# Kernel optimization log

Hardware: AMD Instinct MI355X
Metric: run time of the kernel (lower is better)

## Reference

```python
import jax, jax.numpy as jnp
import numpy as np

B, T, N, P2, K_S = 8, 64, 128, 256, 64

def setup_inputs() -> dict:
    key = jax.random.key(0)
    k1, k2, k3, k4 = jax.random.split(key, 4)
    x = jax.random.normal(k1, (B, T, N, P2), dtype=jnp.float32)
    W_Q = jax.random.uniform(k2, (P2, K_S), dtype=jnp.float32)
    W_K = jax.random.uniform(k3, (P2, K_S), dtype=jnp.float32)
    W_V = jax.random.uniform(k4, (P2, P2), dtype=jnp.float32)
    return {"x": x, "W_Q": W_Q, "W_K": W_K, "W_V": W_V}

def reference(x, W_Q, W_K, W_V):
    # x: [B, T, N, P2]
    q = jnp.einsum('btnp,pk->btnk', x, W_Q)          # [B,T,N,K_S]
    k = jnp.einsum('btnp,pk->btnk', x, W_K)          # [B,T,N,K_S]
    v = jnp.einsum('btnp,pq->btnq', x, W_V)          # [B,T,N,P2]
    scale = jnp.sqrt(jnp.asarray(K_S, dtype=x.dtype))
    scores = jnp.einsum('btik,btjk->btij', q, k) / scale  # [B,T,N,N]
    # NOTE: original uses nn.Softmax(dim=1) -> softmax over the T axis.
    attn = jax.nn.softmax(scores, axis=1)
    return jnp.einsum('btij,btjq->btiq', attn, v)    # [B,T,N,P2]
```

## Files before the change

### kernel.cpp

```cpp
#include <hip/hip_runtime.h>
#include <hip/hip_bf16.h>

#define Bv 8
#define Tv 64
#define Nv 128
#define P2v 256
#define KSv 64

typedef __attribute__((ext_vector_type(8))) short bf8;
typedef __attribute__((ext_vector_type(4))) float f4;

#define MFMA16(a, b, c) __builtin_amdgcn_mfma_f32_16x16x32_bf16((a), (b), (c), 0, 0, 0)

__device__ __forceinline__ unsigned short f2bf(float f) {
  unsigned u = __float_as_uint(f);
  return (unsigned short)((u + 0x7fffu + ((u >> 16) & 1u)) >> 16);
}
__device__ __forceinline__ float bf2f(unsigned short h) {
  return __uint_as_float(((unsigned)h) << 16);
}

__device__ __forceinline__ int swz64(int r, int c) {
  return r * 64 + ((((c >> 3)) ^ (r & 7)) << 3) + (c & 7);
}
__device__ __forceinline__ int swz32(int r, int c) {
  return r * 32 + ((((c >> 3)) ^ (r & 3)) << 3) + (c & 7);
}
__device__ __forceinline__ int swz128(int r, int c) {
  return r * 128 + ((((c >> 3)) ^ (r & 7)) << 3) + (c & 7);
}

__global__ __launch_bounds__(256) void prep_w_kernel(
    const float* __restrict__ Wq, const float* __restrict__ Wk,
    const float* __restrict__ Wv, unsigned short* __restrict__ wqh,
    unsigned short* __restrict__ wql, unsigned short* __restrict__ wkh,
    unsigned short* __restrict__ wkl, unsigned short* __restrict__ wvf) {
  const int e = blockIdx.x * 256 + threadIdx.x;
  if (e < 32768) {
    const float* W = (e < 16384) ? Wq : Wk;
    unsigned short* oh = (e < 16384) ? wqh : wkh;
    unsigned short* ol = (e < 16384) ? wql : wkl;
    const int t = e & 16383;
    const int jj = t & 7, lane = (t >> 3) & 63, nt = (t >> 9) & 3, pt = t >> 11;
    const int p = pt * 32 + 8 * (lane >> 4) + jj;
    const int n = nt * 16 + (lane & 15);
    const float v = W[p * KSv + n];
    const unsigned short h = f2bf(v);
    oh[t] = h;
    ol[t] = f2bf(v - bf2f(h));
  } else {
    const int t = e - 32768;
    const int jj = t & 7, lane = (t >> 3) & 63, nt = (t >> 9) & 15, pt = t >> 13;
    const int p = pt * 32 + 8 * (lane >> 4) + jj;
    const int q = nt * 16 + (lane & 15);
    wvf[t] = f2bf(Wv[p * P2v + q]);
  }
}

__global__ __launch_bounds__(512) void qk_kernel(
    const float* __restrict__ x, const unsigned short* __restrict__ wqh,
    const unsigned short* __restrict__ wql,
    const unsigned short* __restrict__ wkh,
    const unsigned short* __restrict__ wkl, float* __restrict__ S) {
  __shared__ alignas(16) unsigned short xh_l[Nv * 32];
  __shared__ alignas(16) unsigned short xl_l[Nv * 32];
  __shared__ alignas(16) unsigned short qh_l[Nv * KSv];
  __shared__ alignas(16) unsigned short ql_l[Nv * KSv];
  __shared__ alignas(16) unsigned short kh_l[Nv * KSv];
  __shared__ alignas(16) unsigned short kl_l[Nv * KSv];
  const int bt = blockIdx.x;
  const float* __restrict__ X = x + (size_t)bt * (Nv * P2v);
  const int tid = threadIdx.x, lane = tid & 63, wid = tid >> 6;
  const int lg = lane >> 4, lr = lane & 15;
  const bool isQ = (wid < 4);
  const int nt = wid & 3;
  const unsigned short* __restrict__ wh = isQ ? wqh : wkh;
  const unsigned short* __restrict__ wl = isQ ? wql : wkl;

  const f4 zero = {0.f, 0.f, 0.f, 0.f};
  f4 acc[8];
#pragma unroll
  for (int rt = 0; rt < 8; ++rt) acc[rt] = zero;

  const int srow = tid >> 2;
  const int sp = (tid & 3) * 8;
  const float* __restrict__ Xrow = X + srow * P2v + sp;

  float4 pv0 = *(const float4*)(Xrow);
  float4 pv1 = *(const float4*)(Xrow + 4);
  bf8 pwh = *(const bf8*)(wh + (nt * 64 + lane) * 8);
  bf8 pwl = *(const bf8*)(wl + (nt * 64 + lane) * 8);

  for (int c = 0; c < 8; ++c) {
    ushort4 h0, l0, h1, l1;
    h0.x = f2bf(pv0.x); l0.x = f2bf(pv0.x - bf2f(h0.x));
    h0.y = f2bf(pv0.y); l0.y = f2bf(pv0.y - bf2f(h0.y));
    h0.z = f2bf(pv0.z); l0.z = f2bf(pv0.z - bf2f(h0.z));
    h0.w = f2bf(pv0.w); l0.w = f2bf(pv0.w - bf2f(h0.w));
    h1.x = f2bf(pv1.x); l1.x = f2bf(pv1.x - bf2f(h1.x));
    h1.y = f2bf(pv1.y); l1.y = f2bf(pv1.y - bf2f(h1.y));
    h1.z = f2bf(pv1.z); l1.z = f2bf(pv1.z - bf2f(h1.z));
    h1.w = f2bf(pv1.w); l1.w = f2bf(pv1.w - bf2f(h1.w));
    const bf8 cwh = pwh, cwl = pwl;

    __syncthreads();
    const int off = swz32(srow, sp);
    *(ushort4*)(xh_l + off) = h0;
    *(ushort4*)(xh_l + off + 4) = h1;
    *(ushort4*)(xl_l + off) = l0;
    *(ushort4*)(xl_l + off + 4) = l1;

    if (c < 7) {
      pv0 = *(const float4*)(Xrow + (c + 1) * 32);
      pv1 = *(const float4*)(Xrow + (c + 1) * 32 + 4);
      const int wo = (((c + 1) * 4 + nt) * 64 + lane) * 8;
      pwh = *(const bf8*)(wh + wo);
      pwl = *(const bf8*)(wl + wo);
    }
    __syncthreads();
#pragma unroll
    for (int rt = 0; rt < 8; ++rt) {
      const int xoff = swz32(rt * 16 + lr, lg * 8);
      const bf8 xh = *(const bf8*)(xh_l + xoff);
      const bf8 xl = *(const bf8*)(xl_l + xoff);
      acc[rt] = MFMA16(xh, cwh, acc[rt]);
      acc[rt] = MFMA16(xh, cwl, acc[rt]);
      acc[rt] = MFMA16(xl, cwh, acc[rt]);
    }
  }

  unsigned short* const oh = isQ ? qh_l : kh_l;
  unsigned short* const ol = isQ ? ql_l : kl_l;
#pragma unroll
  for (int rt = 0; rt < 8; ++rt) {
#pragma unroll
    for (int rr = 0; rr < 4; ++rr) {
      const int i = rt * 16 + 4 * lg + rr;
      const int ks = nt * 16 + lr;
      const int off = swz64(i, ks);
      const float v = acc[rt][rr];
      const unsigned short h = f2bf(v);
      oh[off] = h;
      ol[off] = f2bf(v - bf2f(h));
    }
  }
  __syncthreads();

  const int r0 = wid * 16;
  f4 aS[8];
#pragma unroll
  for (int n = 0; n < 8; ++n) aS[n] = zero;
#pragma unroll
  for (int kt2 = 0; kt2 < 2; ++kt2) {
    const int qoff = swz64(r0 + lr, kt2 * 32 + lg * 8);
    const bf8 fqh = *(const bf8*)(qh_l + qoff);
    const bf8 fql = *(const bf8*)(ql_l + qoff);
#pragma unroll
    for (int n = 0; n < 8; ++n) {
      const int koff = swz64(n * 16 + lr, kt2 * 32 + lg * 8);
      const bf8 fkh = *(const bf8*)(kh_l + koff);
      const bf8 fkl = *(const bf8*)(kl_l + koff);
      aS[n] = MFMA16(fqh, fkh, aS[n]);
      aS[n] = MFMA16(fqh, fkl, aS[n]);
      aS[n] = MFMA16(fql, fkh, aS[n]);
    }
  }
  float* __restrict__ Sb = S + (size_t)bt * (Nv * Nv);
#pragma unroll
  for (int n = 0; n < 8; ++n) {
#pragma unroll
    for (int rr = 0; rr < 4; ++rr) {
      Sb[(r0 + 4 * lg + rr) * Nv + n * 16 + lr] = aS[n][rr] * 0.125f;
    }
  }
}

__global__ __launch_bounds__(256) void softmax_t_kernel(
    const float* __restrict__ S, unsigned short* __restrict__ Abf) {
  const int idx = blockIdx.x * 256 + threadIdx.x;
  const int j = idx & (Nv - 1);
  const int i = (idx >> 7) & (Nv - 1);
  const int b = idx >> 14;
  const size_t base = ((size_t)b * Tv * Nv * Nv) + (size_t)i * Nv + j;

  float vals[Tv];
  float m = -1e30f;
#pragma unroll
  for (int t = 0; t < Tv; ++t) {
    const float v = S[base + (size_t)t * Nv * Nv];
    vals[t] = v;
    m = fmaxf(m, v);
  }
  float s = 0.f;
#pragma unroll
  for (int t = 0; t < Tv; ++t) {
    const float e = __expf(vals[t] - m);
    vals[t] = e;
    s += e;
  }
  const float inv = 1.f / s;
#pragma unroll
  for (int t = 0; t < Tv; ++t) {
    Abf[base + (size_t)t * Nv * Nv] = f2bf(vals[t] * inv);
  }
}

__global__ __launch_bounds__(512) void av_kernel(
    const float* __restrict__ x, const unsigned short* __restrict__ wvf,
    const unsigned short* __restrict__ Abf, float* __restrict__ out) {
  __shared__ alignas(16) unsigned short xa[Nv * KSv];
  __shared__ alignas(16) unsigned short vth[Nv * Nv];
  const int bt = blockIdx.x;
  const float* __restrict__ X = x + (size_t)bt * (Nv * P2v);
  const unsigned short* __restrict__ Ab = Abf + (size_t)bt * (Nv * Nv);
  float* __restrict__ ob = out + (size_t)bt * (Nv * P2v);
  const int tid = threadIdx.x, lane = tid & 63, wid = tid >> 6;
  const int lg = lane >> 4, lr = lane & 15;
  const int r0 = wid * 16;

  bf8 af[4];
#pragma unroll
  for (int kt = 0; kt < 4; ++kt) {
    af[kt] = *(const bf8*)(Ab + (r0 + lr) * Nv + kt * 32 + lg * 8);
  }

  const f4 zero = {0.f, 0.f, 0.f, 0.f};
  f4 aV[16];
#pragma unroll
  for (int n = 0; n < 16; ++n) aV[n] = zero;

  const int srow = tid >> 4;
  const int sp = (tid & 15) * 4;
  const float* __restrict__ Xrow = X + srow * P2v + sp;

  float4 pf0 = *(const float4*)(Xrow);
  float4 pf1 = *(const float4*)(Xrow + 32 * P2v);
  float4 pf2 = *(const float4*)(Xrow + 64 * P2v);
  float4 pf3 = *(const float4*)(Xrow + 96 * P2v);

  for (int c = 0; c < 4; ++c) {
    ushort4 q0, q1, q2, q3;
    q0.x = f2bf(pf0.x); q0.y = f2bf(pf0.y); q0.z = f2bf(pf0.z); q0.w = f2bf(pf0.w);
    q1.x = f2bf(pf1.x); q1.y = f2bf(pf1.y); q1.z = f2bf(pf1.z); q1.w = f2bf(pf1.w);
    q2.x = f2bf(pf2.x); q2.y = f2bf(pf2.y); q2.z = f2bf(pf2.z); q2.w = f2bf(pf2.w);
    q3.x = f2bf(pf3.x); q3.y = f2bf(pf3.y); q3.z = f2bf(pf3.z); q3.w = f2bf(pf3.w);

    __syncthreads();
    *(ushort4*)(xa + swz64(srow, sp)) = q0;
    *(ushort4*)(xa + swz64(srow + 32, sp)) = q1;
    *(ushort4*)(xa + swz64(srow + 64, sp)) = q2;
    *(ushort4*)(xa + swz64(srow + 96, sp)) = q3;

    if (c < 3) {
      pf0 = *(const float4*)(Xrow + (c + 1) * 64);
      pf1 = *(const float4*)(Xrow + (c + 1) * 64 + 32 * P2v);
      pf2 = *(const float4*)(Xrow + (c + 1) * 64 + 64 * P2v);
      pf3 = *(const float4*)(Xrow + (c + 1) * 64 + 96 * P2v);
    }
    __syncthreads();
#pragma unroll
    for (int ktl = 0; ktl < 2; ++ktl) {
      const int kt = c * 2 + ktl;
#pragma unroll
      for (int h = 0; h < 2; ++h) {
        const int ntile = h * 8 + wid;
        const int o = ((kt * 16 + ntile) * 64 + lane) * 8;
        const bf8 fv = *(const bf8*)(wvf + o);
#pragma unroll
        for (int rt = 0; rt < 8; ++rt) {
          const bf8 xh =
              *(const bf8*)(xa + swz64(rt * 16 + lr, ktl * 32 + lg * 8));
          aV[h * 8 + rt] = MFMA16(xh, fv, aV[h * 8 + rt]);
        }
      }
    }
  }

#pragma unroll
  for (int h = 0; h < 2; ++h) {
    if (h == 1) __syncthreads();
    const int ql = wid * 16 + lr;
#pragma unroll
    for (int rt = 0; rt < 8; ++rt) {
      const int j0 = rt * 16 + 4 * lg;
      ushort4 pk;
      pk.x = f2bf(aV[h * 8 + rt][0]);
      pk.y = f2bf(aV[h * 8 + rt][1]);
      pk.z = f2bf(aV[h * 8 + rt][2]);
      pk.w = f2bf(aV[h * 8 + rt][3]);
      *(ushort4*)(vth + swz128(ql, j0)) = pk;
    }
    __syncthreads();

    f4 aO[8];
#pragma unroll
    for (int n = 0; n < 8; ++n) aO[n] = zero;
#pragma unroll
    for (int kt = 0; kt < 4; ++kt) {
#pragma unroll
      for (int n = 0; n < 8; ++n) {
        const bf8 vf =
            *(const bf8*)(vth + swz128(n * 16 + lr, kt * 32 + lg * 8));
        aO[n] = MFMA16(af[kt], vf, aO[n]);
      }
    }
#pragma unroll
    for (int n = 0; n < 8; ++n) {
#pragma unroll
      for (int rr = 0; rr < 4; ++rr) {
        ob[(r0 + 4 * lg + rr) * P2v + h * 128 + n * 16 + lr] = aO[n][rr];
      }
    }
  }
}

extern "C" void kernel_launch(void* const* d_in, const int* in_sizes, int n_in,
                              void* d_out, int out_size, void* d_ws,
                              size_t ws_size, hipStream_t stream) {
  const float* x = (const float*)d_in[0];
  const float* Wq = (const float*)d_in[1];
  const float* Wk = (const float*)d_in[2];
  const float* Wv = (const float*)d_in[3];
  float* out = (float*)d_out;

  unsigned short* wqh = (unsigned short*)d_ws;
  unsigned short* wql = wqh + 16384;
  unsigned short* wkh = wql + 16384;
  unsigned short* wkl = wkh + 16384;
  unsigned short* wvf = wkl + 16384;
  float* S = (float*)((char*)d_ws + 262144);
  unsigned short* Abf = (unsigned short*)((char*)d_ws + 262144 + 33554432);

  hipLaunchKernelGGL(prep_w_kernel, dim3(384), dim3(256), 0, stream, Wq, Wk,
                     Wv, wqh, wql, wkh, wkl, wvf);
  hipLaunchKernelGGL(qk_kernel, dim3(Bv * Tv), dim3(512), 0, stream, x, wqh,
                     wql, wkh, wkl, S);
  hipLaunchKernelGGL(softmax_t_kernel, dim3(Bv * Nv * Nv / 256), dim3(256), 0,
                     stream, S, Abf);
  hipLaunchKernelGGL(av_kernel, dim3(Bv * Tv), dim3(512), 0, stream, x, wvf,
                     Abf, out);
}
```

Before: 80.53 us.

## Cache bf16 x from QK kernel and use direct-load AV kernel

The QK kernel now also writes the bf16 high part of x to a workspace buffer. A new AV kernel reads that bf16 copy straight from global memory as MFMA fragments, instead of reloading fp32 x and staging it through shared memory. This halves the bytes read for x in the AV stage and frees shared memory, at the cost of an extra 16MB write in the QK kernel. It also makes uncoalesced, strided fragment loads from global memory. The new path only runs when the workspace is large enough, otherwise the old kernel is used.

```diff
diff --git a/kernel.cpp b/kernel.cpp
--- a/kernel.cpp
+++ b/kernel.cpp
@@ -61,7 +61,8 @@
     const float* __restrict__ x, const unsigned short* __restrict__ wqh,
     const unsigned short* __restrict__ wql,
     const unsigned short* __restrict__ wkh,
-    const unsigned short* __restrict__ wkl, float* __restrict__ S) {
+    const unsigned short* __restrict__ wkl, float* __restrict__ S,
+    unsigned short* __restrict__ Xh) {
   __shared__ alignas(16) unsigned short xh_l[Nv * 32];
   __shared__ alignas(16) unsigned short xl_l[Nv * 32];
   __shared__ alignas(16) unsigned short qh_l[Nv * KSv];
@@ -85,6 +86,8 @@
   const int srow = tid >> 2;
   const int sp = (tid & 3) * 8;
   const float* __restrict__ Xrow = X + srow * P2v + sp;
+  unsigned short* __restrict__ XhRow =
+      Xh ? (Xh + (size_t)(bt * Nv + srow) * P2v + sp) : (unsigned short*)0;
 
   float4 pv0 = *(const float4*)(Xrow);
   float4 pv1 = *(const float4*)(Xrow + 4);
@@ -103,6 +106,11 @@
     h1.w = f2bf(pv1.w); l1.w = f2bf(pv1.w - bf2f(h1.w));
     const bf8 cwh = pwh, cwl = pwl;
 
+    if (XhRow) {
+      *(ushort4*)(XhRow + c * 32) = h0;
+      *(ushort4*)(XhRow + c * 32 + 4) = h1;
+    }
+
     __syncthreads();
     const int off = swz32(srow, sp);
     *(ushort4*)(xh_l + off) = h0;
@@ -202,6 +210,80 @@
 #pragma unroll
   for (int t = 0; t < Tv; ++t) {
     Abf[base + (size_t)t * Nv * Nv] = f2bf(vals[t] * inv);
+  }
+}
+
+__global__ __launch_bounds__(512) void av_direct_kernel(
+    const unsigned short* __restrict__ Xh,
+    const unsigned short* __restrict__ wvf,
+    const unsigned short* __restrict__ Abf, float* __restrict__ out) {
+  __shared__ alignas(16) unsigned short vth[Nv * Nv];
+  const int bt = blockIdx.x;
+  const unsigned short* __restrict__ Xb = Xh + (size_t)bt * (Nv * P2v);
+  const unsigned short* __restrict__ Ab = Abf + (size_t)bt * (Nv * Nv);
+  float* __restrict__ ob = out + (size_t)bt * (Nv * P2v);
+  const int tid = threadIdx.x, lane = tid & 63, wid = tid >> 6;
+  const int lg = lane >> 4, lr = lane & 15;
+  const int r0 = wid * 16;
+
+  const f4 zero = {0.f, 0.f, 0.f, 0.f};
+  f4 aV[16];
+#pragma unroll
+  for (int n = 0; n < 16; ++n) aV[n] = zero;
+
+#pragma unroll
+  for (int kt = 0; kt < 8; ++kt) {
+    const bf8 fv0 = *(const bf8*)(wvf + ((kt * 16 + wid) * 64 + lane) * 8);
+    const bf8 fv1 = *(const bf8*)(wvf + ((kt * 16 + 8 + wid) * 64 + lane) * 8);
+#pragma unroll
+    for (int rt = 0; rt < 8; ++rt) {
+      const bf8 xf = *(const bf8*)(Xb + (rt * 16 + lr) * P2v + kt * 32 + lg * 8);
+      aV[rt] = MFMA16(xf, fv0, aV[rt]);
+      aV[8 + rt] = MFMA16(xf, fv1, aV[8 + rt]);
+    }
+  }
+
+  bf8 af[4];
+#pragma unroll
+  for (int kt = 0; kt < 4; ++kt) {
+    af[kt] = *(const bf8*)(Ab + (r0 + lr) * Nv + kt * 32 + lg * 8);
+  }
+
+#pragma unroll
+  for (int h = 0; h < 2; ++h) {
+    if (h == 1) __syncthreads();
+    const int ql = wid * 16 + lr;
+#pragma unroll
+    for (int rt = 0; rt < 8; ++rt) {
+      const int j0 = rt * 16 + 4 * lg;
+      ushort4 pk;
+      pk.x = f2bf(aV[h * 8 + rt][0]);
+      pk.y = f2bf(aV[h * 8 + rt][1]);
+      pk.z = f2bf(aV[h * 8 + rt][2]);
+      pk.w = f2bf(aV[h * 8 + rt][3]);
+      *(ushort4*)(vth + swz128(ql, j0)) = pk;
+    }
+    __syncthreads();
+
+    f4 aO[8];
+#pragma unroll
+    for (int n = 0; n < 8; ++n) aO[n] = zero;
+#pragma unroll
+    for (int kt = 0; kt < 4; ++kt) {
+#pragma unroll
+      for (int n = 0; n < 8; ++n) {
+        const bf8 vf =
+            *(const bf8*)(vth + swz128(n * 16 + lr, kt * 32 + lg * 8));
+        aO[n] = MFMA16(af[kt], vf, aO[n]);
+      }
+    }
+#pragma unroll
+    for (int n = 0; n < 8; ++n) {
+#pragma unroll
+      for (int rr = 0; rr < 4; ++rr) {
+        ob[(r0 + 4 * lg + rr) * P2v + h * 128 + n * 16 + lr] = aO[n][rr];
+      }
+    }
   }
 }
 
@@ -330,13 +412,22 @@
   unsigned short* wvf = wkl + 16384;
   float* S = (float*)((char*)d_ws + 262144);
   unsigned short* Abf = (unsigned short*)((char*)d_ws + 262144 + 33554432);
+  unsigned short* Xh =
+      (unsigned short*)((char*)d_ws + 262144 + 33554432 + 16777216);
+  const size_t need_big = 262144ull + 33554432ull + 16777216ull + 33554432ull;
+  const bool big = (ws_size >= need_big);
 
   hipLaunchKernelGGL(prep_w_kernel, dim3(384), dim3(256), 0, stream, Wq, Wk,
                      Wv, wqh, wql, wkh, wkl, wvf);
   hipLaunchKernelGGL(qk_kernel, dim3(Bv * Tv), dim3(512), 0, stream, x, wqh,
-                     wql, wkh, wkl, S);
+                     wql, wkh, wkl, S, big ? Xh : (unsigned short*)0);
   hipLaunchKernelGGL(softmax_t_kernel, dim3(Bv * Nv * Nv / 256), dim3(256), 0,
                      stream, S, Abf);
-  hipLaunchKernelGGL(av_kernel, dim3(Bv * Tv), dim3(512), 0, stream, x, wvf,
-                     Abf, out);
-}
+  if (big) {
+    hipLaunchKernelGGL(av_direct_kernel, dim3(Bv * Tv), dim3(512), 0, stream,
+                       Xh, wvf, Abf, out);
+  } else {
+    hipLaunchKernelGGL(av_kernel, dim3(Bv * Tv), dim3(512), 0, stream, x, wvf,
+                       Abf, out);
+  }
+}
```

After: 97.32 us. 20.8% more time.
